# Performance work log

Measured on AMD Instinct MI355X. Metric: run time of the kernel, lower is better.

The kernel has to match this reference:

```python
import jax, jax.numpy as jnp
import numpy as np

N = 50000
E = 1600000
IN_C, H1, H2 = 512, 512, 256
N_CLASSES = 40
CENTER_NUM = 8
D_CAT = 2 * H2  # 512


def setup_inputs() -> dict:
    key = jax.random.key(0)
    ks = jax.random.split(key, 9)
    x = jax.random.normal(ks[0], (N, IN_C), dtype=jnp.float32)
    edge_index = jax.random.randint(ks[1], (2, E), 0, N, dtype=jnp.int64)
    s1 = 1.0 / np.sqrt(IN_C)
    s2 = 1.0 / np.sqrt(H1)
    sp = 1.0 / np.sqrt(D_CAT)
    W1 = jax.random.uniform(ks[2], (IN_C, H1), jnp.float32, -s1, s1)
    b1 = jnp.zeros((H1,), jnp.float32)
    W2 = jax.random.uniform(ks[3], (H1, H2), jnp.float32, -s2, s2)
    b2 = jnp.zeros((H2,), jnp.float32)
    Wp = jax.random.uniform(ks[4], (CENTER_NUM, D_CAT), jnp.float32, -sp, sp)   # interior_prototype weight [C, D]
    We = jax.random.uniform(ks[5], (CENTER_NUM, N_CLASSES, D_CAT), jnp.float32, -sp, sp)  # border prototypes
    return {"x": x, "edge_index": edge_index, "W1": W1, "b1": b1, "W2": W2, "b2": b2, "Wp": Wp, "We": We}


def _gcn_conv(x, W, b, src, dst, n):
    # PyG GCNConv: h = xW; out[i] = sum_j norm_ij h[j] + b, with self-loops,
    # norm_ij = deg_i^{-1/2} deg_j^{-1/2}, deg includes self-loop.
    h = x @ W
    ones = jnp.ones(src.shape[0], x.dtype)
    deg = jax.ops.segment_sum(ones, dst, num_segments=n) + 1.0
    dinv = deg ** -0.5
    norm = dinv[src] * dinv[dst]
    agg = jax.ops.segment_sum(h[src] * norm[:, None], dst, num_segments=n)
    agg = agg + h * (dinv * dinv)[:, None]  # self-loop term
    return agg + b


def _mean_aggr(x, src, dst, n):
    # PyG default message x_j with aggr='mean' (custom message_func kwarg is ignored by PyG)
    cnt = jax.ops.segment_sum(jnp.ones(src.shape[0], x.dtype), dst, num_segments=n)
    s = jax.ops.segment_sum(x[src], dst, num_segments=n)
    return s / jnp.maximum(cnt, 1.0)[:, None]


def reference(x, edge_index, W1, b1, W2, b2, Wp, We):
    src, dst = edge_index[0], edge_index[1]
    n = x.shape[0]
    h = jax.nn.relu(_gcn_conv(x, W1, b1, src, dst, n))
    h = _gcn_conv(h, W2, b2, src, dst, n)
    neighbor = _mean_aggr(h, src, dst, n)
    xc = jnp.concatenate([h, neighbor], axis=1)  # [N, 2*H2]
    scores = xc @ Wp.T                            # [N, C]
    idx = jnp.argmax(scores, axis=1)              # [N]
    # all-expert logits then per-node select (same math as masked per-cluster linear)
    all_out = jnp.einsum('nd,ckd->nck', xc, We)   # [N, C, n_classes]
    out = jnp.take_along_axis(all_out, idx[:, None, None], axis=1)[:, 0, :]
    return out, xc
```

## Files before the change

### kernel.cpp

```cpp
#include <hip/hip_runtime.h>
#include <hip/hip_bf16.h>
#include <hip/hip_fp16.h>
#include <cstdint>
#include <cstddef>


using short8 = __attribute__((ext_vector_type(8))) short;
using half8  = __attribute__((ext_vector_type(8))) _Float16;
using f32x4  = __attribute__((ext_vector_type(4))) float;
typedef unsigned char uchar;

#define GLB_AS __attribute__((address_space(1)))
#define LDS_AS __attribute__((address_space(3)))

__device__ inline void unpack_fma_u(uint32_t v, float w, float* a) {
    a[0] = fmaf(w, (float)(v & 0xffu),         a[0]);
    a[1] = fmaf(w, (float)((v >> 8) & 0xffu),  a[1]);
    a[2] = fmaf(w, (float)((v >> 16) & 0xffu), a[2]);
    a[3] = fmaf(w, (float)(v >> 24),           a[3]);
}

__device__ inline half8 dequant8(uint2 raw, float s) {
    const float off = -128.f * s;
    half8 r;
    r[0] = (_Float16)fmaf(s, (float)(raw.x & 0xffu), off);
    r[1] = (_Float16)fmaf(s, (float)((raw.x >> 8) & 0xffu), off);
    r[2] = (_Float16)fmaf(s, (float)((raw.x >> 16) & 0xffu), off);
    r[3] = (_Float16)fmaf(s, (float)(raw.x >> 24), off);
    r[4] = (_Float16)fmaf(s, (float)(raw.y & 0xffu), off);
    r[5] = (_Float16)fmaf(s, (float)((raw.y >> 8) & 0xffu), off);
    r[6] = (_Float16)fmaf(s, (float)((raw.y >> 16) & 0xffu), off);
    r[7] = (_Float16)fmaf(s, (float)(raw.y >> 24), off);
    return r;
}

__global__ __launch_bounds__(256) void prep_kernel(
    const float* __restrict__ x, uchar* __restrict__ xq, float* __restrict__ scale,
    const float* __restrict__ W1, __half* __restrict__ W1T,
    const float* __restrict__ W2, __half* __restrict__ W2T,
    const float* __restrict__ We, __half* __restrict__ We_h,
    int* __restrict__ bcur, int* __restrict__ ecur,
    int n, int nbuck, int cap) {
    const int t = threadIdx.x;
    int b = blockIdx.x;
    const int BXQ = (n + 3) / 4;
    const int BW1 = (512 * 512) / 256;
    const int BW2 = (512 * 256) / 256;
    const int BWe = (8 * 40 * 512) / 256;
    if (b < BXQ) {
        const int node = b * 4 + (t >> 6);
        const int lane = t & 63;
        if (node < n) {
            const float* row = x + (size_t)node * 512;
            const float4 v0 = *(const float4*)&row[lane * 8];
            const float4 v1 = *(const float4*)&row[lane * 8 + 4];
            float m = fmaxf(fmaxf(fmaxf(fabsf(v0.x), fabsf(v0.y)), fmaxf(fabsf(v0.z), fabsf(v0.w))),
                            fmaxf(fmaxf(fabsf(v1.x), fabsf(v1.y)), fmaxf(fabsf(v1.z), fabsf(v1.w))));
#pragma unroll
            for (int off = 32; off; off >>= 1) m = fmaxf(m, __shfl_xor(m, off));
            m = fmaxf(m, 1e-30f);
            const float qs = 127.f / m;
            const int q0 = __float2int_rn(v0.x * qs) + 128, q1 = __float2int_rn(v0.y * qs) + 128;
            const int q2 = __float2int_rn(v0.z * qs) + 128, q3 = __float2int_rn(v0.w * qs) + 128;
            const int q4 = __float2int_rn(v1.x * qs) + 128, q5 = __float2int_rn(v1.y * qs) + 128;
            const int q6 = __float2int_rn(v1.z * qs) + 128, q7 = __float2int_rn(v1.w * qs) + 128;
            uint2 pk;
            pk.x = q0 | (q1 << 8) | (q2 << 16) | (q3 << 24);
            pk.y = q4 | (q5 << 8) | (q6 << 16) | (q7 << 24);
            *(uint2*)&xq[(size_t)node * 512 + lane * 8] = pk;
            if (lane == 0) scale[node] = m / 127.f;
        }
        return;
    }
    b -= BXQ;
    if (b < BW1) {
        const int gid = b * 256 + t;
        const int k = gid >> 9, nn = gid & 511;
        W1T[(size_t)nn * 512 + k] = __float2half(W1[gid]);
        return;
    }
    b -= BW1;
    if (b < BW2) {
        const int gid = b * 256 + t;
        const int k = gid >> 8, nn = gid & 255;
        W2T[(size_t)nn * 512 + k] = __float2half(W2[gid]);
        return;
    }
    b -= BW2;
    if (b < BWe) {
        const int gid = b * 256 + t;
        We_h[gid] = __float2half(We[gid]);
        return;
    }
    if (t < nbuck) bcur[t] = t * cap;
    if (t < 8) ecur[t] = 0;
}

__global__ __launch_bounds__(256) void bucketA_kernel(const int* __restrict__ src,
                                                      const int* __restrict__ dst,
                                                      int* __restrict__ bcur,
                                                      uint32_t* __restrict__ ebuf, int e) {
    __shared__ uint32_t sbuf[4096];
    __shared__ int h[128], gb[128], c2[128];
    const int t = threadIdx.x;
    if (t < 128) { h[t] = 0; c2[t] = 0; }
    __syncthreads();
    const int base = blockIdx.x * 4096;
    const int m = min(4096, e - base);
    for (int j = t; j < m; j += 256) {
        const int s = src[base + j];
        const int d = dst[base + j];
        sbuf[j] = ((uint32_t)s << 16) | (uint32_t)d;
        atomicAdd(&h[d >> 9], 1);
    }
    __syncthreads();
    if (t < 128 && h[t] > 0) gb[t] = atomicAdd(&bcur[t], h[t]);
    __syncthreads();
    for (int j = t; j < m; j += 256) {
        const uint32_t pf = sbuf[j];
        const int b = (int)((pf & 0xFFFFu) >> 9);
        const int r = atomicAdd(&c2[b], 1);
        ebuf[gb[b] + r] = pf;
    }
}

__global__ __launch_bounds__(256) void bucketB_kernel(const uint32_t* __restrict__ ebuf,
                                                      const int* __restrict__ bcur,
                                                      const float* __restrict__ scale,
                                                      int* __restrict__ offsets,
                                                      int* __restrict__ counts,
                                                      float* __restrict__ dinv,
                                                      float* __restrict__ dsc,
                                                      int* __restrict__ ssrc,
                                                      int n, int cap) {
    __shared__ int h[512];
    __shared__ int lofs[512];
    __shared__ int sc[256];
    const int t = threadIdx.x;
    const int b = blockIdx.x;
    const int nbase = b * 512;
    const int nb = min(512, n - nbase);
    h[t] = 0; h[t + 256] = 0;
    __syncthreads();
    const int ebeg = b * cap;
    const int ecount = bcur[b] - ebeg;
    for (int j = t; j < ecount; j += 256)
        atomicAdd(&h[ebuf[ebeg + j] & 511u], 1);
    __syncthreads();
    const int pair = h[2 * t] + h[2 * t + 1];
    sc[t] = pair;
    __syncthreads();
    for (int off = 1; off < 256; off <<= 1) {
        const int u = (t >= off) ? sc[t - off] : 0;
        __syncthreads();
        sc[t] += u;
        __syncthreads();
    }
    const int pbase = sc[t] - pair;
    lofs[2 * t] = pbase;
    lofs[2 * t + 1] = pbase + h[2 * t];
    __syncthreads();
    for (int j = t; j < nb; j += 256) {
        const int cnt = h[j];
        const float dv = rsqrtf((float)cnt + 1.0f);
        offsets[nbase + j] = ebeg + lofs[j];
        counts[nbase + j] = cnt;
        dinv[nbase + j] = dv;
        dsc[nbase + j] = dv * scale[nbase + j];
    }
    __syncthreads();
    lofs[2 * t] += ebeg;
    lofs[2 * t + 1] += ebeg;
    __syncthreads();
    for (int j = t; j < ecount; j += 256) {
        const uint32_t pf = ebuf[ebeg + j];
        const int d = (int)(pf & 511u);
        const int s = (int)(pf >> 16);
        const int pos = atomicAdd(&lofs[d], 1);
        ssrc[pos] = s;
    }
}

__global__ __launch_bounds__(256) void agg512_kernel(const uchar* __restrict__ xq,
                                                     const int* __restrict__ ssrc,
                                                     const int* __restrict__ offsets,
                                                     const int* __restrict__ counts,
                                                     const float* __restrict__ dinv,
                                                     const float* __restrict__ dsc,
                                                     __half* __restrict__ A16, int n) {
    const int lane = threadIdx.x & 63;
    const int node = (blockIdx.x * blockDim.x + threadIdx.x) >> 6;
    if (node >= n) return;
    const int beg = offsets[node];
    const int end = beg + counts[node];
    const float di = dinv[node];
    const int half = lane >> 5;
    const int hl = lane & 31;
    float acc[16];
#pragma unroll
    for (int j = 0; j < 16; ++j) acc[j] = 0.f;
    float wsum = 0.f;

    for (int b0 = beg; b0 < end; b0 += 64) {
        const int idx = b0 + lane;
        const int sl = (idx < end) ? ssrc[idx] : 0;
        const float wl = (idx < end) ? di * dsc[sl] : 0.f;
        const int m = min(64, end - b0);
#pragma unroll 8
        for (int kp = 0; kp < m; kp += 2) {
            const int k = kp + half;
            const int s = __shfl(sl, k);
            const float w = __shfl(wl, k);
            wsum += w;
            const uint4 raw = *(const uint4*)&xq[(size_t)s * 512 + hl * 16];
            unpack_fma_u(raw.x, w, &acc[0]);
            unpack_fma_u(raw.y, w, &acc[4]);
            unpack_fma_u(raw.z, w, &acc[8]);
            unpack_fma_u(raw.w, w, &acc[12]);
        }
    }
#pragma unroll
    for (int j = 0; j < 16; ++j) acc[j] += __shfl(acc[j], hl + 32);
    wsum += __shfl(wsum, hl + 32);

    if (half == 0) {
        const float w = di * dsc[node];
        wsum += w;
        const uint4 raw = *(const uint4*)&xq[(size_t)node * 512 + hl * 16];
        unpack_fma_u(raw.x, w, &acc[0]);
        unpack_fma_u(raw.y, w, &acc[4]);
        unpack_fma_u(raw.z, w, &acc[8]);
        unpack_fma_u(raw.w, w, &acc[12]);
#pragma unroll
        for (int j = 0; j < 16; ++j) acc[j] = fmaf(-128.f, wsum, acc[j]);
        float4 pk0, pk1;
        *(__half2*)&pk0.x = __floats2half2_rn(acc[0], acc[1]);
        *(__half2*)&pk0.y = __floats2half2_rn(acc[2], acc[3]);
        *(__half2*)&pk0.z = __floats2half2_rn(acc[4], acc[5]);
        *(__half2*)&pk0.w = __floats2half2_rn(acc[6], acc[7]);
        *(__half2*)&pk1.x = __floats2half2_rn(acc[8], acc[9]);
        *(__half2*)&pk1.y = __floats2half2_rn(acc[10], acc[11]);
        *(__half2*)&pk1.z = __floats2half2_rn(acc[12], acc[13]);
        *(__half2*)&pk1.w = __floats2half2_rn(acc[14], acc[15]);
        *(float4*)&A16[(size_t)node * 512 + hl * 16] = pk0;
        *(float4*)&A16[(size_t)node * 512 + hl * 16 + 8] = pk1;
    }
}

__global__ __launch_bounds__(256) void tquant_kernel(const __half* __restrict__ t16,
                                                     const float* __restrict__ dinv,
                                                     uchar* __restrict__ tq,
                                                     float* __restrict__ dts, int n) {
    const int lane = threadIdx.x & 63;
    const int node = (blockIdx.x * blockDim.x + threadIdx.x) >> 6;
    if (node >= n) return;
    const float2 raw = *(const float2*)&t16[(size_t)node * 256 + lane * 4];
    const float2 f0 = __half22float2(*(const __half2*)&raw.x);
    const float2 f1 = __half22float2(*(const __half2*)&raw.y);
    float m = fmaxf(fmaxf(fabsf(f0.x), fabsf(f0.y)), fmaxf(fabsf(f1.x), fabsf(f1.y)));
#pragma unroll
    for (int off = 32; off; off >>= 1) m = fmaxf(m, __shfl_xor(m, off));
    m = fmaxf(m, 1e-30f);
    const float qs = 127.f / m;
    const int q0 = __float2int_rn(f0.x * qs) + 128, q1 = __float2int_rn(f0.y * qs) + 128;
    const int q2 = __float2int_rn(f1.x * qs) + 128, q3 = __float2int_rn(f1.y * qs) + 128;
    const uint32_t pk = q0 | (q1 << 8) | (q2 << 16) | (q3 << 24);
    *(uint32_t*)&tq[(size_t)node * 256 + lane * 4] = pk;
    if (lane == 0) dts[node] = dinv[node] * (m / 127.f);
}

__global__ __launch_bounds__(256) void agg256_kernel(const uchar* __restrict__ tq,
                                                     const int* __restrict__ ssrc,
                                                     const int* __restrict__ offsets,
                                                     const int* __restrict__ counts,
                                                     const float* __restrict__ dinv,
                                                     const float* __restrict__ dts,
                                                     const float* __restrict__ bias,
                                                     float* __restrict__ xc,
                                                     uchar* __restrict__ hq8,
                                                     float* __restrict__ hsc, int n) {
    const int lane = threadIdx.x & 63;
    const int node = (blockIdx.x * blockDim.x + threadIdx.x) >> 6;
    if (node >= n) return;
    const int beg = offsets[node];
    const int end = beg + counts[node];
    const float di = dinv[node];
    const int q = lane >> 4;
    const int ql = lane & 15;
    float acc[16];
#pragma unroll
    for (int j = 0; j < 16; ++j) acc[j] = 0.f;
    float wsum = 0.f;

    for (int b0 = beg; b0 < end; b0 += 64) {
        const int idx = b0 + lane;
        const int sl = (idx < end) ? ssrc[idx] : 0;
        const float wl = (idx < end) ? di * dts[sl] : 0.f;
        const int m = min(64, end - b0);
#pragma unroll 4
        for (int kp = 0; kp < m; kp += 4) {
            const int k = kp + q;
            const int s = __shfl(sl, k);
            const float w = __shfl(wl, k);
            wsum += w;
            const uint4 raw = *(const uint4*)&tq[(size_t)s * 256 + ql * 16];
            unpack_fma_u(raw.x, w, &acc[0]);
            unpack_fma_u(raw.y, w, &acc[4]);
            unpack_fma_u(raw.z, w, &acc[8]);
            unpack_fma_u(raw.w, w, &acc[12]);
        }
    }
#pragma unroll
    for (int j = 0; j < 16; ++j) acc[j] += __shfl(acc[j], lane + 32);
    wsum += __shfl(wsum, lane + 32);
#pragma unroll
    for (int j = 0; j < 16; ++j) acc[j] += __shfl(acc[j], lane + 16);
    wsum += __shfl(wsum, lane + 16);

    if (q == 0) {
        const float w = di * dts[node];
        wsum += w;
        const uint4 raw = *(const uint4*)&tq[(size_t)node * 256 + ql * 16];
        unpack_fma_u(raw.x, w, &acc[0]);
        unpack_fma_u(raw.y, w, &acc[4]);
        unpack_fma_u(raw.z, w, &acc[8]);
        unpack_fma_u(raw.w, w, &acc[12]);
#pragma unroll
        for (int j = 0; j < 16; ++j) acc[j] = fmaf(-128.f, wsum, acc[j]);
#pragma unroll
        for (int i = 0; i < 4; ++i) {
            const float4 bv = *(const float4*)&bias[ql * 16 + i * 4];
            acc[i * 4 + 0] += bv.x; acc[i * 4 + 1] += bv.y;
            acc[i * 4 + 2] += bv.z; acc[i * 4 + 3] += bv.w;
        }
#pragma unroll
        for (int i = 0; i < 4; ++i)
            *(float4*)&xc[(size_t)node * 512 + ql * 16 + i * 4] =
                make_float4(acc[i * 4 + 0], acc[i * 4 + 1], acc[i * 4 + 2], acc[i * 4 + 3]);
        float am = 0.f;
#pragma unroll
        for (int j = 0; j < 16; ++j) am = fmaxf(am, fabsf(acc[j]));
#pragma unroll
        for (int off = 1; off < 16; off <<= 1) am = fmaxf(am, __shfl_xor(am, off));
        am = fmaxf(am, 1e-30f);
        const float qs = 127.f / am;
        uint32_t pk[4];
#pragma unroll
        for (int i = 0; i < 4; ++i) {
            const int a0 = __float2int_rn(acc[i * 4 + 0] * qs) + 128;
            const int a1 = __float2int_rn(acc[i * 4 + 1] * qs) + 128;
            const int a2 = __float2int_rn(acc[i * 4 + 2] * qs) + 128;
            const int a3 = __float2int_rn(acc[i * 4 + 3] * qs) + 128;
            pk[i] = a0 | (a1 << 8) | (a2 << 16) | (a3 << 24);
        }
        *(uint4*)&hq8[(size_t)node * 256 + ql * 16] = *(uint4*)pk;
        if (ql == 0) hsc[node] = am / 127.f;
    }
}

template <int EPI>
__global__ __launch_bounds__(256) void gemm_f16_kernel(
    const __half* __restrict__ A, const __half* __restrict__ WT,
    const float* __restrict__ bias, __half* __restrict__ C,
    int M, int N, int K, int ldc) {
    __shared__ ushort smem[2 * 4096];
    const int tid = threadIdx.x;
    const int lane = tid & 63;
    const int w = tid >> 6;
    const int wr = w >> 1, wc = w & 1;
    const int bm = blockIdx.y * 128;
    const int bn = blockIdx.x * 128;

    f32x4 acc[4][4];
#pragma unroll
    for (int i = 0; i < 4; ++i)
#pragma unroll
        for (int j = 0; j < 4; ++j) acc[i][j] = f32x4{0.f, 0.f, 0.f, 0.f};

    for (int k0 = 0; k0 < K; k0 += 32) {
        __syncthreads();
#pragma unroll
        for (int i = 0; i < 4; ++i) {
            const int q = w * 4 + i;
            const bool isA = q < 8;
            const int seg = (isA ? q : q - 8) * 64 + lane;
            const int row = seg >> 2;
            const int kc = (seg & 3) * 8;
            int grow = (isA ? bm : bn) + row;
            grow = min(grow, (isA ? M : N) - 1);
            const ushort* g = (const ushort*)(isA ? A : WT) + (size_t)grow * K + k0 + kc;
            __builtin_amdgcn_global_load_lds((const GLB_AS void*)g,
                                             (LDS_AS void*)(smem + q * 512), 16, 0, 0);
        }
        __syncthreads();

        const int koff = (lane >> 4) * 8;
        const int rsel = lane & 15;
        half8 a[4], b[4];
#pragma unroll
        for (int f = 0; f < 4; ++f) {
            const int ar = wr * 64 + f * 16 + rsel;
            a[f] = __builtin_bit_cast(half8, *(const short8*)&smem[ar * 32 + koff]);
            const int bc = wc * 64 + f * 16 + rsel;
            b[f] = __builtin_bit_cast(half8, *(const short8*)&smem[4096 + bc * 32 + koff]);
        }
#pragma unroll
        for (int i = 0; i < 4; ++i)
#pragma unroll
            for (int j = 0; j < 4; ++j)
                acc[i][j] = __builtin_amdgcn_mfma_f32_16x16x32_f16(a[i], b[j], acc[i][j], 0, 0, 0);
    }

    const int crow0 = wr * 64 + (lane >> 4) * 4;
    const int ccol0 = wc * 64 + (lane & 15);
#pragma unroll
    for (int f = 0; f < 4; ++f) {
#pragma unroll
        for (int g = 0; g < 4; ++g) {
            const int colg = bn + ccol0 + g * 16;
            float bv = 0.f;
            if constexpr (EPI == 1) bv = bias[colg];
#pragma unroll
            for (int j = 0; j < 4; ++j) {
                const int rowg = bm + crow0 + f * 16 + j;
                if (rowg >= M) continue;
                float v = acc[f][g][j];
                if constexpr (EPI == 1) v = fmaxf(v + bv, 0.f);
                C[(size_t)rowg * ldc + colg] = __float2half(v);
            }
        }
    }
}

__global__ __launch_bounds__(256) void mean_score_kernel(const int* __restrict__ ssrc,
                                                         const int* __restrict__ offsets,
                                                         const int* __restrict__ counts,
                                                         const float* __restrict__ Wp,
                                                         const uchar* __restrict__ hq8,
                                                         const float* __restrict__ hsc,
                                                         float* __restrict__ xc,
                                                         uchar* __restrict__ mq8,
                                                         float* __restrict__ msc,
                                                         int* __restrict__ bidx, int n) {
    __shared__ float lds_f[4][512];
    const int lane = threadIdx.x & 63;
    const int w = threadIdx.x >> 6;
    const int node = (blockIdx.x * blockDim.x + threadIdx.x) >> 6;
    if (node >= n) return;
    const int beg = offsets[node];
    const int cnt = counts[node];
    const int end = beg + cnt;
    const int c0 = lane * 4;
    const int q = lane >> 4;
    const int ql = lane & 15;

    float acc[16];
#pragma unroll
    for (int j = 0; j < 16; ++j) acc[j] = 0.f;
    float wsum = 0.f;
    for (int b0 = beg; b0 < end; b0 += 64) {
        const int idx = b0 + lane;
        const int sl = (idx < end) ? ssrc[idx] : 0;
        const float wl = (idx < end) ? hsc[sl] : 0.f;
        const int m = min(64, end - b0);
#pragma unroll 4
        for (int kp = 0; kp < m; kp += 4) {
            const int k = kp + q;
            const int s = __shfl(sl, k);
            const float ww = __shfl(wl, k);
            wsum += ww;
            const uint4 raw = *(const uint4*)&hq8[(size_t)s * 256 + ql * 16];
            unpack_fma_u(raw.x, ww, &acc[0]);
            unpack_fma_u(raw.y, ww, &acc[4]);
            unpack_fma_u(raw.z, ww, &acc[8]);
            unpack_fma_u(raw.w, ww, &acc[12]);
        }
    }
#pragma unroll
    for (int j = 0; j < 16; ++j) acc[j] += __shfl(acc[j], lane + 32);
    wsum += __shfl(wsum, lane + 32);
#pragma unroll
    for (int j = 0; j < 16; ++j) acc[j] += __shfl(acc[j], lane + 16);
    wsum += __shfl(wsum, lane + 16);

    const float inv = 1.f / fmaxf((float)cnt, 1.f);
    if (q == 0) {
#pragma unroll
        for (int j = 0; j < 16; ++j) acc[j] = fmaf(-128.f, wsum, acc[j]) * inv;
#pragma unroll
        for (int i = 0; i < 4; ++i) {
            const float4 v = make_float4(acc[i * 4 + 0], acc[i * 4 + 1], acc[i * 4 + 2], acc[i * 4 + 3]);
            *(float4*)&xc[(size_t)node * 512 + 256 + ql * 16 + i * 4] = v;
            *(float4*)&lds_f[w][256 + ql * 16 + i * 4] = v;
        }
        float am = 0.f;
#pragma unroll
        for (int j = 0; j < 16; ++j) am = fmaxf(am, fabsf(acc[j]));
#pragma unroll
        for (int off = 1; off < 16; off <<= 1) am = fmaxf(am, __shfl_xor(am, off));
        am = fmaxf(am, 1e-30f);
        const float qs = 127.f / am;
        uint32_t pk[4];
#pragma unroll
        for (int i = 0; i < 4; ++i) {
            const int a0 = __float2int_rn(acc[i * 4 + 0] * qs) + 128;
            const int a1 = __float2int_rn(acc[i * 4 + 1] * qs) + 128;
            const int a2 = __float2int_rn(acc[i * 4 + 2] * qs) + 128;
            const int a3 = __float2int_rn(acc[i * 4 + 3] * qs) + 128;
            pk[i] = a0 | (a1 << 8) | (a2 << 16) | (a3 << 24);
        }
        *(uint4*)&mq8[(size_t)node * 256 + ql * 16] = *(uint4*)pk;
        if (ql == 0) msc[node] = am / 127.f;
    }
    const float4 a = *(const float4*)&xc[(size_t)node * 512 + c0];
    *(float4*)&lds_f[w][c0] = a;

    const int r = lane & 15;
    const int quad = lane >> 4;

    float av[32];
#pragma unroll
    for (int i = 0; i < 8; ++i) {
        const int jj = (i + r) & 7;
        *(float4*)&av[i * 4] = *(const float4*)&lds_f[w][r * 32 + jj * 4];
    }

    float s0, s1;
#pragma unroll
    for (int t = 0; t < 2; ++t) {
        const int c = t * 4 + quad;
        const float* wp = &Wp[c * 512 + r * 32];
        float p = 0.f;
#pragma unroll
        for (int i = 0; i < 8; ++i) {
            const int jj = (i + r) & 7;
            const float4 wv = *(const float4*)&wp[jj * 4];
            p = fmaf(av[i * 4 + 0], wv.x, p);
            p = fmaf(av[i * 4 + 1], wv.y, p);
            p = fmaf(av[i * 4 + 2], wv.z, p);
            p = fmaf(av[i * 4 + 3], wv.w, p);
        }
        p += __shfl_xor(p, 1); p += __shfl_xor(p, 2);
        p += __shfl_xor(p, 4); p += __shfl_xor(p, 8);
        if (t == 0) s0 = p; else s1 = p;
    }
    float best = -3.0e38f;
    int be = 0;
#pragma unroll
    for (int c = 0; c < 8; ++c) {
        const float v = __shfl((c < 4) ? s0 : s1, (c & 3) * 16);
        if (v > best) { best = v; be = c; }
    }
    if (lane == 0) bidx[node] = be;
}

__global__ __launch_bounds__(256) void bucket_scatter_kernel(const int* __restrict__ bidx,
                                                             int* __restrict__ cursor,
                                                             int* __restrict__ elist, int n) {
    __shared__ int h[8], base[8], c2[8];
    const int t = threadIdx.x;
    if (t < 8) { h[t] = 0; c2[t] = 0; }
    __syncthreads();
    const int i = blockIdx.x * 256 + t;
    int b = 0;
    if (i < n) {
        b = bidx[i];
        atomicAdd(&h[b], 1);
    }
    __syncthreads();
    if (t < 8) base[t] = (h[t] > 0) ? atomicAdd(&cursor[t], h[t]) : 0;
    __syncthreads();
    if (i < n) {
        const int r = atomicAdd(&c2[b], 1);
        elist[(size_t)b * n + base[b] + r] = i;
    }
}

__global__ __launch_bounds__(256) void expert_gemm_kernel(
    const int* __restrict__ elist, const int* __restrict__ ecnt,
    const uchar* __restrict__ hq8, const float* __restrict__ hsc,
    const uchar* __restrict__ mq8, const float* __restrict__ msc,
    const __half* __restrict__ We_h, float* __restrict__ out, int n) {
    const int e = blockIdx.x;
    const int cnt = ecnt[e];
    const int base = blockIdx.y * 128;
    if (base >= cnt) return;
    __shared__ __half Bs[40][520];
    const int tid = threadIdx.x;
#pragma unroll
    for (int i = 0; i < 10; ++i) {
        const int seg = tid + i * 256;
        const int br = seg >> 6;
        const int bc = (seg & 63) * 8;
        *(float4*)&Bs[br][bc] = *(const float4*)&We_h[((size_t)e * 40 + br) * 512 + bc];
    }
    __syncthreads();

    const int w = tid >> 6, lane = tid & 63;
    const int rsel = lane & 15, koff = (lane >> 4) * 8;
    const int grow0 = base + w * 32 + rsel;
    const int grow1 = grow0 + 16;
    const int i0 = elist[(size_t)e * n + min(grow0, cnt - 1)];
    const int i1 = elist[(size_t)e * n + min(grow1, cnt - 1)];
    const float hs0 = hsc[i0], ms0 = msc[i0];
    const float hs1 = hsc[i1], ms1 = msc[i1];

    f32x4 acc[2][3];
#pragma unroll
    for (int mf = 0; mf < 2; ++mf)
#pragma unroll
        for (int nf = 0; nf < 3; ++nf) acc[mf][nf] = f32x4{0.f, 0.f, 0.f, 0.f};

#pragma unroll
    for (int ks = 0; ks < 16; ++ks) {
        const int k0 = ks * 32 + koff;
        const bool lo = ks < 8;
        const uchar* p0 = lo ? &hq8[(size_t)i0 * 256 + k0] : &mq8[(size_t)i0 * 256 + (k0 - 256)];
        const uchar* p1 = lo ? &hq8[(size_t)i1 * 256 + k0] : &mq8[(size_t)i1 * 256 + (k0 - 256)];
        const half8 a0 = dequant8(*(const uint2*)p0, lo ? hs0 : ms0);
        const half8 a1 = dequant8(*(const uint2*)p1, lo ? hs1 : ms1);
#pragma unroll
        for (int nf = 0; nf < 3; ++nf) {
            const int brow = min(nf * 16 + rsel, 39);
            const half8 b = __builtin_bit_cast(half8, *(const short8*)&Bs[brow][ks * 32 + koff]);
            acc[0][nf] = __builtin_amdgcn_mfma_f32_16x16x32_f16(a0, b, acc[0][nf], 0, 0, 0);
            acc[1][nf] = __builtin_amdgcn_mfma_f32_16x16x32_f16(a1, b, acc[1][nf], 0, 0, 0);
        }
    }

    const int crow = (lane >> 4) * 4;
    const int ccol = lane & 15;
#pragma unroll
    for (int mf = 0; mf < 2; ++mf) {
#pragma unroll
        for (int nf = 0; nf < 3; ++nf) {
            const int col = nf * 16 + ccol;
            if (col >= 40) continue;
#pragma unroll
            for (int j = 0; j < 4; ++j) {
                const int gr = base + w * 32 + mf * 16 + crow + j;
                if (gr >= cnt) continue;
                const int node = elist[(size_t)e * n + gr];
                out[(size_t)node * 40 + col] = acc[mf][nf][j];
            }
        }
    }
}

extern "C" void kernel_launch(void* const* d_in, const int* in_sizes, int n_in,
                              void* d_out, int out_size, void* d_ws, size_t ws_size,
                              hipStream_t stream) {
    const float* x  = (const float*)d_in[0];
    const int*  edge = (const int*)d_in[1];
    const float* W1 = (const float*)d_in[2];
    const float* b1 = (const float*)d_in[3];
    const float* W2 = (const float*)d_in[4];
    const float* b2 = (const float*)d_in[5];
    const float* Wp = (const float*)d_in[6];
    const float* We = (const float*)d_in[7];

    const int n = in_sizes[0] / 512;
    const int e = in_sizes[1] / 2;
    const int* src = edge;
    const int* dst = edge + e;

    const int nbuck = (n + 511) / 512;
    const int cap = 20480;

    char* ws = (char*)d_ws;
    __half* A16 = (__half*)ws;
    __half* t16 = (__half*)ws;
    uchar*  mq8 = (uchar*)ws;
    char* p = ws + (size_t)n * 512 * 2;
    __half* h1 = (__half*)p;
    uchar* tq8 = (uchar*)p;
    uchar* hq8 = (uchar*)p + (size_t)n * 256;
    p += (size_t)n * 512 * 2;
    uchar* xq = (uchar*)p; p += (size_t)n * 512;
    __half* W1T = (__half*)p; p += 512 * 512 * 2;
    __half* W2T = (__half*)p; p += 256 * 512 * 2;
    __half* We_h = (__half*)p; p += 8 * 40 * 512 * 2;
    auto align16 = [](size_t v) { return (v + 15) & ~(size_t)15; };
    float* scale = (float*)p;   p += align16((size_t)n * 4);
    float* dinv = (float*)p;    p += align16((size_t)n * 4);
    float* dsc = (float*)p;     p += align16((size_t)n * 4);
    float* dts = (float*)p;     p += align16((size_t)n * 4);
    float* hsc = (float*)p;     p += align16((size_t)n * 4);
    float* msc = (float*)p;     p += align16((size_t)n * 4);
    int* counts = (int*)p;      p += align16((size_t)n * 4);
    int* offsets = (int*)p;     p += align16((size_t)n * 4);
    int* bidx = (int*)p;        p += align16((size_t)n * 4);
    int* bcur = (int*)p;        p += align16((size_t)nbuck * 4);
    int* ecur = (int*)p;        p += align16((size_t)8 * 4);
    int* elist = (int*)p;       p += align16((size_t)8 * n * 4);
    uint32_t* ebuf = (uint32_t*)p; p += align16((size_t)nbuck * cap * 4);
    int* ssrc = (int*)p;

    float* out = (float*)d_out;
    float* xc = (float*)d_out + (size_t)n * 40;

    const int prep_blocks = (n + 3) / 4 + (512 * 512) / 256 +
                            (512 * 256) / 256 + (8 * 40 * 512) / 256 + 1;
    prep_kernel<<<prep_blocks, 256, 0, stream>>>(x, xq, scale, W1, W1T, W2, W2T, We, We_h,
                                                 bcur, ecur, n, nbuck, cap);

    bucketA_kernel<<<(e + 4095) / 4096, 256, 0, stream>>>(src, dst, bcur, ebuf, e);
    bucketB_kernel<<<nbuck, 256, 0, stream>>>(ebuf, bcur, scale, offsets, counts, dinv, dsc,
                                              ssrc, n, cap);

    const int waves_grid = (n * 64 + 255) / 256;
    agg512_kernel<<<waves_grid, 256, 0, stream>>>(xq, ssrc, offsets, counts, dinv, dsc, A16, n);
    dim3 g1(512 / 128, (n + 127) / 128);
    gemm_f16_kernel<1><<<g1, 256, 0, stream>>>(A16, W1T, b1, h1, n, 512, 512, 512);

    dim3 g2(256 / 128, (n + 127) / 128);
    gemm_f16_kernel<0><<<g2, 256, 0, stream>>>(h1, W2T, nullptr, t16, n, 256, 512, 256);
    tquant_kernel<<<waves_grid, 256, 0, stream>>>(t16, dinv, tq8, dts, n);

    agg256_kernel<<<waves_grid, 256, 0, stream>>>(tq8, ssrc, offsets, counts, dinv, dts, b2,
                                                  xc, hq8, hsc, n);

    mean_score_kernel<<<waves_grid, 256, 0, stream>>>(ssrc, offsets, counts, Wp, hq8, hsc,
                                                      xc, mq8, msc, bidx, n);

    bucket_scatter_kernel<<<(n + 255) / 256, 256, 0, stream>>>(bidx, ecur, elist, n);

    dim3 ge(8, (n + 127) / 128);
    expert_gemm_kernel<<<ge, 256, 0, stream>>>(elist, ecur, hq8, hsc, mq8, msc, We_h, out, n);
}
```

Measured before the change: 551.3 us.

## Fuse second GEMM with per-row int8 quantization in a full-width tile

```diff
diff --git a/kernel.cpp b/kernel.cpp
--- a/kernel.cpp
+++ b/kernel.cpp
@@ -247,26 +247,179 @@
     }
 }
 
-__global__ __launch_bounds__(256) void tquant_kernel(const __half* __restrict__ t16,
-                                                     const float* __restrict__ dinv,
-                                                     uchar* __restrict__ tq,
-                                                     float* __restrict__ dts, int n) {
-    const int lane = threadIdx.x & 63;
-    const int node = (blockIdx.x * blockDim.x + threadIdx.x) >> 6;
-    if (node >= n) return;
-    const float2 raw = *(const float2*)&t16[(size_t)node * 256 + lane * 4];
-    const float2 f0 = __half22float2(*(const __half2*)&raw.x);
-    const float2 f1 = __half22float2(*(const __half2*)&raw.y);
-    float m = fmaxf(fmaxf(fabsf(f0.x), fabsf(f0.y)), fmaxf(fabsf(f1.x), fabsf(f1.y)));
-#pragma unroll
-    for (int off = 32; off; off >>= 1) m = fmaxf(m, __shfl_xor(m, off));
-    m = fmaxf(m, 1e-30f);
-    const float qs = 127.f / m;
-    const int q0 = __float2int_rn(f0.x * qs) + 128, q1 = __float2int_rn(f0.y * qs) + 128;
-    const int q2 = __float2int_rn(f1.x * qs) + 128, q3 = __float2int_rn(f1.y * qs) + 128;
-    const uint32_t pk = q0 | (q1 << 8) | (q2 << 16) | (q3 << 24);
-    *(uint32_t*)&tq[(size_t)node * 256 + lane * 4] = pk;
-    if (lane == 0) dts[node] = dinv[node] * (m / 127.f);
+__global__ __launch_bounds__(256) void gemm1_kernel(
+    const __half* __restrict__ A, const __half* __restrict__ WT,
+    const float* __restrict__ bias, __half* __restrict__ C,
+    int M, int N, int K, int ldc) {
+    __shared__ ushort smem[2 * 4096];
+    const int tid = threadIdx.x;
+    const int lane = tid & 63;
+    const int w = tid >> 6;
+    const int wr = w >> 1, wc = w & 1;
+    const int bm = blockIdx.y * 128;
+    const int bn = blockIdx.x * 128;
+
+    f32x4 acc[4][4];
+#pragma unroll
+    for (int i = 0; i < 4; ++i)
+#pragma unroll
+        for (int j = 0; j < 4; ++j) acc[i][j] = f32x4{0.f, 0.f, 0.f, 0.f};
+
+    for (int k0 = 0; k0 < K; k0 += 32) {
+        __syncthreads();
+#pragma unroll
+        for (int i = 0; i < 4; ++i) {
+            const int q = w * 4 + i;
+            const bool isA = q < 8;
+            const int seg = (isA ? q : q - 8) * 64 + lane;
+            const int row = seg >> 2;
+            const int kc = (seg & 3) * 8;
+            int grow = (isA ? bm : bn) + row;
+            grow = min(grow, (isA ? M : N) - 1);
+            const ushort* g = (const ushort*)(isA ? A : WT) + (size_t)grow * K + k0 + kc;
+            __builtin_amdgcn_global_load_lds((const GLB_AS void*)g,
+                                             (LDS_AS void*)(smem + q * 512), 16, 0, 0);
+        }
+        __syncthreads();
+
+        const int koff = (lane >> 4) * 8;
+        const int rsel = lane & 15;
+        half8 a[4], b[4];
+#pragma unroll
+        for (int f = 0; f < 4; ++f) {
+            const int ar = wr * 64 + f * 16 + rsel;
+            a[f] = __builtin_bit_cast(half8, *(const short8*)&smem[ar * 32 + koff]);
+            const int bc = wc * 64 + f * 16 + rsel;
+            b[f] = __builtin_bit_cast(half8, *(const short8*)&smem[4096 + bc * 32 + koff]);
+        }
+#pragma unroll
+        for (int i = 0; i < 4; ++i)
+#pragma unroll
+            for (int j = 0; j < 4; ++j)
+                acc[i][j] = __builtin_amdgcn_mfma_f32_16x16x32_f16(a[i], b[j], acc[i][j], 0, 0, 0);
+    }
+
+    const int crow0 = wr * 64 + (lane >> 4) * 4;
+    const int ccol0 = wc * 64 + (lane & 15);
+#pragma unroll
+    for (int f = 0; f < 4; ++f) {
+#pragma unroll
+        for (int g = 0; g < 4; ++g) {
+            const int colg = bn + ccol0 + g * 16;
+            const float bv = bias[colg];
+#pragma unroll
+            for (int j = 0; j < 4; ++j) {
+                const int rowg = bm + crow0 + f * 16 + j;
+                if (rowg >= M) continue;
+                const float v = fmaxf(acc[f][g][j] + bv, 0.f);
+                C[(size_t)rowg * ldc + colg] = __float2half(v);
+            }
+        }
+    }
+}
+
+__global__ __launch_bounds__(512) void gemm2q_kernel(
+    const __half* __restrict__ A,
+    const __half* __restrict__ WT,
+    const float* __restrict__ dinv,
+    uchar* __restrict__ tq, float* __restrict__ dts, int M) {
+    constexpr int K = 512, N = 256;
+    __shared__ ushort smem[3 * 4096];
+    __shared__ float ldsm[4][128];
+    const int tid = threadIdx.x;
+    const int lane = tid & 63;
+    const int w = tid >> 6;
+    const int wr = w >> 2, wc = w & 3;
+    const int bm = blockIdx.x * 128;
+
+    f32x4 acc[4][4];
+#pragma unroll
+    for (int i = 0; i < 4; ++i)
+#pragma unroll
+        for (int j = 0; j < 4; ++j) acc[i][j] = f32x4{0.f, 0.f, 0.f, 0.f};
+
+    for (int k0 = 0; k0 < K; k0 += 32) {
+        __syncthreads();
+#pragma unroll
+        for (int i = 0; i < 3; ++i) {
+            const int q = w * 3 + i;
+            const bool isA = q < 8;
+            const int seg = (isA ? q : q - 8) * 64 + lane;
+            const int row = seg >> 2;
+            const int kc = (seg & 3) * 8;
+            int grow = isA ? min(bm + row, M - 1) : row;
+            const ushort* g = (const ushort*)(isA ? A : WT) + (size_t)grow * K + k0 + kc;
+            __builtin_amdgcn_global_load_lds((const GLB_AS void*)g,
+                                             (LDS_AS void*)(smem + q * 512), 16, 0, 0);
+        }
+        __syncthreads();
+
+        const int koff = (lane >> 4) * 8;
+        const int rsel = lane & 15;
+        half8 a[4], b[4];
+#pragma unroll
+        for (int f = 0; f < 4; ++f) {
+            const int ar = wr * 64 + f * 16 + rsel;
+            a[f] = __builtin_bit_cast(half8, *(const short8*)&smem[ar * 32 + koff]);
+            const int bc = wc * 64 + f * 16 + rsel;
+            b[f] = __builtin_bit_cast(half8, *(const short8*)&smem[4096 + bc * 32 + koff]);
+        }
+#pragma unroll
+        for (int i = 0; i < 4; ++i)
+#pragma unroll
+            for (int j = 0; j < 4; ++j)
+                acc[i][j] = __builtin_amdgcn_mfma_f32_16x16x32_f16(a[i], b[j], acc[i][j], 0, 0, 0);
+    }
+
+    const int quad = lane >> 4;
+    const int rsel = lane & 15;
+    float am[4][4];
+#pragma unroll
+    for (int f = 0; f < 4; ++f)
+#pragma unroll
+        for (int j = 0; j < 4; ++j) {
+            float m = fmaxf(fmaxf(fabsf(acc[f][0][j]), fabsf(acc[f][1][j])),
+                            fmaxf(fabsf(acc[f][2][j]), fabsf(acc[f][3][j])));
+            m = fmaxf(m, __shfl_xor(m, 1));
+            m = fmaxf(m, __shfl_xor(m, 2));
+            m = fmaxf(m, __shfl_xor(m, 4));
+            m = fmaxf(m, __shfl_xor(m, 8));
+            am[f][j] = m;
+        }
+    if (rsel == 0) {
+#pragma unroll
+        for (int f = 0; f < 4; ++f)
+#pragma unroll
+            for (int j = 0; j < 4; ++j)
+                ldsm[wc][wr * 64 + f * 16 + quad * 4 + j] = am[f][j];
+    }
+    __syncthreads();
+    if (tid < 128) {
+        const int node = bm + tid;
+        if (node < M) {
+            const float m = fmaxf(fmaxf(ldsm[0][tid], ldsm[1][tid]),
+                                  fmaxf(ldsm[2][tid], ldsm[3][tid]));
+            dts[node] = dinv[node] * (fmaxf(m, 1e-30f) / 127.f);
+        }
+    }
+#pragma unroll
+    for (int f = 0; f < 4; ++f) {
+#pragma unroll
+        for (int j = 0; j < 4; ++j) {
+            const int rl = wr * 64 + f * 16 + quad * 4 + j;
+            const int row = bm + rl;
+            if (row >= M) continue;
+            const float m = fmaxf(fmaxf(ldsm[0][rl], ldsm[1][rl]),
+                                  fmaxf(ldsm[2][rl], ldsm[3][rl]));
+            const float qs = 127.f / fmaxf(m, 1e-30f);
+#pragma unroll
+            for (int g = 0; g < 4; ++g) {
+                const int col = wc * 64 + g * 16 + rsel;
+                const int q = __float2int_rn(acc[f][g][j] * qs) + 128;
+                tq[(size_t)row * 256 + col] = (uchar)q;
+            }
+        }
+    }
 }
 
 __global__ __launch_bounds__(256) void agg256_kernel(const uchar* __restrict__ tq,
@@ -355,80 +508,6 @@
         }
         *(uint4*)&hq8[(size_t)node * 256 + ql * 16] = *(uint4*)pk;
         if (ql == 0) hsc[node] = am / 127.f;
-    }
-}
-
-template <int EPI>
-__global__ __launch_bounds__(256) void gemm_f16_kernel(
-    const __half* __restrict__ A, const __half* __restrict__ WT,
-    const float* __restrict__ bias, __half* __restrict__ C,
-    int M, int N, int K, int ldc) {
-    __shared__ ushort smem[2 * 4096];
-    const int tid = threadIdx.x;
-    const int lane = tid & 63;
-    const int w = tid >> 6;
-    const int wr = w >> 1, wc = w & 1;
-    const int bm = blockIdx.y * 128;
-    const int bn = blockIdx.x * 128;
-
-    f32x4 acc[4][4];
-#pragma unroll
-    for (int i = 0; i < 4; ++i)
-#pragma unroll
-        for (int j = 0; j < 4; ++j) acc[i][j] = f32x4{0.f, 0.f, 0.f, 0.f};
-
-    for (int k0 = 0; k0 < K; k0 += 32) {
-        __syncthreads();
-#pragma unroll
-        for (int i = 0; i < 4; ++i) {
-            const int q = w * 4 + i;
-            const bool isA = q < 8;
-            const int seg = (isA ? q : q - 8) * 64 + lane;
-            const int row = seg >> 2;
-            const int kc = (seg & 3) * 8;
-            int grow = (isA ? bm : bn) + row;
-            grow = min(grow, (isA ? M : N) - 1);
-            const ushort* g = (const ushort*)(isA ? A : WT) + (size_t)grow * K + k0 + kc;
-            __builtin_amdgcn_global_load_lds((const GLB_AS void*)g,
-                                             (LDS_AS void*)(smem + q * 512), 16, 0, 0);
-        }
-        __syncthreads();
-
-        const int koff = (lane >> 4) * 8;
-        const int rsel = lane & 15;
-        half8 a[4], b[4];
-#pragma unroll
-        for (int f = 0; f < 4; ++f) {
-            const int ar = wr * 64 + f * 16 + rsel;
-            a[f] = __builtin_bit_cast(half8, *(const short8*)&smem[ar * 32 + koff]);
-            const int bc = wc * 64 + f * 16 + rsel;
-            b[f] = __builtin_bit_cast(half8, *(const short8*)&smem[4096 + bc * 32 + koff]);
-        }
-#pragma unroll
-        for (int i = 0; i < 4; ++i)
-#pragma unroll
-            for (int j = 0; j < 4; ++j)
-                acc[i][j] = __builtin_amdgcn_mfma_f32_16x16x32_f16(a[i], b[j], acc[i][j], 0, 0, 0);
-    }
-
-    const int crow0 = wr * 64 + (lane >> 4) * 4;
-    const int ccol0 = wc * 64 + (lane & 15);
-#pragma unroll
-    for (int f = 0; f < 4; ++f) {
-#pragma unroll
-        for (int g = 0; g < 4; ++g) {
-            const int colg = bn + ccol0 + g * 16;
-            float bv = 0.f;
-            if constexpr (EPI == 1) bv = bias[colg];
-#pragma unroll
-            for (int j = 0; j < 4; ++j) {
-                const int rowg = bm + crow0 + f * 16 + j;
-                if (rowg >= M) continue;
-                float v = acc[f][g][j];
-                if constexpr (EPI == 1) v = fmaxf(v + bv, 0.f);
-                C[(size_t)rowg * ldc + colg] = __float2half(v);
-            }
-        }
     }
 }
 
@@ -669,12 +748,11 @@
 
     char* ws = (char*)d_ws;
     __half* A16 = (__half*)ws;
-    __half* t16 = (__half*)ws;
-    uchar*  mq8 = (uchar*)ws;
+    uchar* tq8 = (uchar*)ws;
+    uchar* mq8 = (uchar*)ws + (size_t)n * 256;
     char* p = ws + (size_t)n * 512 * 2;
     __half* h1 = (__half*)p;
-    uchar* tq8 = (uchar*)p;
-    uchar* hq8 = (uchar*)p + (size_t)n * 256;
+    uchar* hq8 = (uchar*)p;
     p += (size_t)n * 512 * 2;
     uchar* xq = (uchar*)p; p += (size_t)n * 512;
     __half* W1T = (__half*)p; p += 512 * 512 * 2;
@@ -711,11 +789,9 @@
     const int waves_grid = (n * 64 + 255) / 256;
     agg512_kernel<<<waves_grid, 256, 0, stream>>>(xq, ssrc, offsets, counts, dinv, dsc, A16, n);
     dim3 g1(512 / 128, (n + 127) / 128);
-    gemm_f16_kernel<1><<<g1, 256, 0, stream>>>(A16, W1T, b1, h1, n, 512, 512, 512);
-
-    dim3 g2(256 / 128, (n + 127) / 128);
-    gemm_f16_kernel<0><<<g2, 256, 0, stream>>>(h1, W2T, nullptr, t16, n, 256, 512, 256);
-    tquant_kernel<<<waves_grid, 256, 0, stream>>>(t16, dinv, tq8, dts, n);
+    gemm1_kernel<<<g1, 256, 0, stream>>>(A16, W1T, b1, h1, n, 512, 512, 512);
+
+    gemm2q_kernel<<<(n + 127) / 128, 512, 0, stream>>>(h1, W2T, dinv, tq8, dts, n);
 
     agg256_kernel<<<waves_grid, 256, 0, stream>>>(tq8, ssrc, offsets, counts, dinv, dts, b2,
                                                   xc, hq8, hsc, n);
```

Result: faster. 531.4 us (-3.6%).
